# Optimization experiments

Hardware: AMD Instinct MI355X
Metric: run time of the kernel (lower is better)

The kernel has to match this reference:

```python
import jax, jax.numpy as jnp
import numpy as np

B, T, W = 128, 256, 256
D, C, K = 128, 256, 12
TEMP = 0.1


def _l2norm(x):
    # matches F.normalize(dim=-1, eps=1e-12)
    return x / jnp.maximum(jnp.linalg.norm(x, axis=-1, keepdims=True), 1e-12)


def setup_inputs() -> dict:
    key = jax.random.key(0)
    ks = jax.random.split(key, 12)
    s = 0.02
    return {
        "rr_windows": jax.random.normal(ks[0], (B, T, W), dtype=jnp.float32),
        # Encoder: 2-layer MLP window->2D->D
        "enc_w1": jax.random.normal(ks[1], (W, 2 * D), dtype=jnp.float32) * s,
        "enc_b1": jnp.zeros((2 * D,), dtype=jnp.float32),
        "enc_w2": jax.random.normal(ks[2], (2 * D, D), dtype=jnp.float32) * s,
        "enc_b2": jnp.zeros((D,), dtype=jnp.float32),
        # ARBlock: single-layer GRU latent->context
        "W_ih": jax.random.normal(ks[3], (3 * C, D), dtype=jnp.float32) * s,
        "W_hh": jax.random.normal(ks[4], (3 * C, C), dtype=jnp.float32) * s,
        "b_ih": jnp.zeros((3 * C,), dtype=jnp.float32),
        "b_hh": jnp.zeros((3 * C,), dtype=jnp.float32),
        # K prediction heads Wk: context->latent
        "Wk_w": jax.random.normal(ks[5], (K, C, D), dtype=jnp.float32) * s,
        "Wk_b": jnp.zeros((K, D), dtype=jnp.float32),
    }


def _gru(z_seq, W_ih, W_hh, b_ih, b_hh):
    # z_seq: [B, T, D] -> c_seq [B, T, C]
    gx = jnp.einsum("btd,gd->btg", z_seq, W_ih) + b_ih  # [B,T,3C]
    gx = jnp.swapaxes(gx, 0, 1)  # [T,B,3C]
    h0 = jnp.zeros((z_seq.shape[0], C), dtype=z_seq.dtype)

    def step(h, gx_t):
        gh = h @ W_hh.T + b_hh
        xr, xz, xn = jnp.split(gx_t, 3, axis=-1)
        hr, hz, hn = jnp.split(gh, 3, axis=-1)
        r = jax.nn.sigmoid(xr + hr)
        zg = jax.nn.sigmoid(xz + hz)
        n = jnp.tanh(xn + r * hn)
        h_new = (1.0 - zg) * n + zg * h
        return h_new, h_new

    _, hs = jax.lax.scan(step, h0, gx)  # [T,B,C]
    return jnp.swapaxes(hs, 0, 1)


def reference(rr_windows, enc_w1, enc_b1, enc_w2, enc_b2, W_ih, W_hh, b_ih, b_hh, Wk_w, Wk_b):
    # Encoder on each window (dropout inactive)
    h = jax.nn.relu(jnp.einsum("btw,wh->bth", rr_windows, enc_w1) + enc_b1)
    z_seq = jnp.einsum("bth,hd->btd", h, enc_w2) + enc_b2  # [B,T,D]
    z_seq = _l2norm(z_seq)
    c_seq = _gru(z_seq, W_ih, W_hh, b_ih, b_hh)  # [B,T,C]

    Tp = T - K
    c_used = c_seq[:, :Tp, :]  # [B,Tp,C]
    # all (t,k) predictions at once: [K,B,Tp,D]
    preds = _l2norm(jnp.einsum("btc,kcd->kbtd", c_used, Wk_w) + Wk_b[:, None, None, :])
    # logits over ALL timesteps; cat([pos, negs-excl-pos]) == full set reordered,
    # so cross_entropy = logsumexp(full) - pos_logit (logsumexp order-invariant)
    logits = jnp.einsum("kbtd,bsd->kbts", preds, z_seq) / TEMP  # [K,B,Tp,T]
    pos_idx = jnp.arange(Tp)[None, :] + jnp.arange(1, K + 1)[:, None]  # [K,Tp]
    pos_logit = jnp.take_along_axis(
        logits, pos_idx[:, None, :, None], axis=-1
    )[..., 0]  # [K,B,Tp]
    avg_loss = jnp.mean(jax.nn.logsumexp(logits, axis=-1) - pos_logit)

    # accuracy: positive beats all negatives (ties to positive, as in argmax w/ pos first)
    is_pos = jnp.arange(T)[None, None, None, :] == pos_idx[:, None, :, None]
    neg_max = jnp.max(jnp.where(is_pos, -jnp.inf, logits), axis=-1)
    avg_accuracy = jnp.mean((pos_logit >= neg_max).astype(jnp.float32)) * 100.0
    return (avg_loss, avg_accuracy, z_seq, c_seq)
```

## Files before the change

### kernel.cpp

```cpp
#include <hip/hip_runtime.h>
#include <stdint.h>


typedef _Float16 f16;
typedef __attribute__((ext_vector_type(2))) _Float16 f16x2;
typedef __attribute__((ext_vector_type(8))) _Float16 f16x8;
typedef __attribute__((ext_vector_type(4))) float f32x4;

__device__ __forceinline__ f16x2 u2h(unsigned int x) { return __builtin_bit_cast(f16x2, x); }
__device__ __forceinline__ float sigm_(float x) { return __builtin_amdgcn_rcpf(1.f + __expf(-x)); }
__device__ __forceinline__ float tanh_(float x) { return 1.f - 2.f * __builtin_amdgcn_rcpf(__expf(2.f * x) + 1.f); }

#define NTOT_LOSS 374784.0f

__global__ void k_prep(const float* __restrict__ w1, const float* __restrict__ w2,
                       const float* __restrict__ wih, const float* __restrict__ whh,
                       const float* __restrict__ wkw,
                       f16* __restrict__ w1T, f16* __restrict__ w2T, f16* __restrict__ wihF,
                       f16* __restrict__ whhF, f16* __restrict__ wkT, float* __restrict__ accb) {
  const int stride = gridDim.x * blockDim.x;
  const int tid = blockIdx.x * blockDim.x + threadIdx.x;
  if (tid == 0) { accb[0] = 0.f; accb[1] = 0.f; }
  for (int i = tid; i < 65536; i += stride) { int n = i >> 8, k = i & 255; w1T[i] = (f16)w1[k * 256 + n]; }
  for (int i = tid; i < 32768; i += stride) { int n = i >> 8, k = i & 255; w2T[i] = (f16)w2[k * 128 + n]; }
  for (int i = tid; i < 98304; i += stride) wihF[i] = (f16)wih[i];
  for (int i = tid; i < 196608; i += stride) whhF[i] = (f16)whh[i];
  for (int i = tid; i < 393216; i += stride) {
    int kk = i >> 15, rem = i & 32767, d = rem >> 8, c = rem & 255;
    wkT[i] = (f16)wkw[(kk << 15) + c * 128 + d];
  }
}

template <int KTOT, bool AF32, bool RELU>
__global__ __launch_bounds__(256) void k_gemm64(const void* __restrict__ Aptr,
                                                const f16* __restrict__ BT,
                                                const float* __restrict__ bias,
                                                f16* __restrict__ out, const int NT) {
  __shared__ __align__(16) f16 Al[64][40];
  __shared__ __align__(16) f16 Bl[64][40];
  const int m0 = blockIdx.x * 64;
  const int n0 = blockIdx.y * 64;
  const int t = threadIdx.x;
  const int w = t >> 6, l = t & 63, lr = l & 15, lg = l >> 4;
  const int arow = t >> 2, akq = (t & 3) * 8;
  f32x4 acc[4] = {};
  for (int ks = 0; ks < KTOT / 32; ++ks) {
    const int kc = ks * 32;
    __syncthreads();
    if constexpr (AF32) {
      const float* src = (const float*)Aptr + (size_t)(m0 + arow) * KTOT + kc + akq;
      float4 v0 = *(const float4*)src;
      float4 v1 = *(const float4*)(src + 4);
      f16x8 hv = {(f16)v0.x, (f16)v0.y, (f16)v0.z, (f16)v0.w,
                  (f16)v1.x, (f16)v1.y, (f16)v1.z, (f16)v1.w};
      *(f16x8*)&Al[arow][akq] = hv;
    } else {
      const f16* src = (const f16*)Aptr + (size_t)(m0 + arow) * KTOT + kc + akq;
      *(f16x8*)&Al[arow][akq] = *(const f16x8*)src;
    }
    *(f16x8*)&Bl[arow][akq] = *(const f16x8*)(BT + (size_t)(n0 + arow) * KTOT + kc + akq);
    __syncthreads();
    f16x8 af = *(const f16x8*)&Al[16 * w + lr][lg * 8];
#pragma unroll
    for (int nt = 0; nt < 4; ++nt) {
      f16x8 bf = *(const f16x8*)&Bl[nt * 16 + lr][lg * 8];
      acc[nt] = __builtin_amdgcn_mfma_f32_16x16x32_f16(af, bf, acc[nt], 0, 0, 0);
    }
  }
#pragma unroll
  for (int nt = 0; nt < 4; ++nt) {
    const int n = n0 + nt * 16 + lr;
    const float bb = bias[n];
#pragma unroll
    for (int r = 0; r < 4; ++r) {
      const int m = m0 + 16 * w + lg * 4 + r;
      float v = acc[nt][r] + bb;
      if (RELU) v = fmaxf(v, 0.f);
      out[(size_t)m * NT + n] = (f16)v;
    }
  }
}

__global__ __launch_bounds__(256) void k_enc2(const f16* __restrict__ A, const f16* __restrict__ BT,
                                              const float* __restrict__ bias,
                                              float* __restrict__ zf32, f16* __restrict__ zf16) {
  __shared__ __align__(16) f16 Al[64][40];
  __shared__ __align__(16) f16 Bl[128][40];
  const int m0 = blockIdx.x * 64;
  const int t = threadIdx.x;
  const int w = t >> 6, l = t & 63, lr = l & 15, lg = l >> 4;
  const int arow = t >> 2, akq = (t & 3) * 8;
  f32x4 acc[8] = {};
  for (int ks = 0; ks < 8; ++ks) {
    const int kc = ks * 32;
    __syncthreads();
    *(f16x8*)&Al[arow][akq] = *(const f16x8*)(A + (size_t)(m0 + arow) * 256 + kc + akq);
#pragma unroll
    for (int hh = 0; hh < 2; ++hh) {
      const int brow = arow + 64 * hh;
      *(f16x8*)&Bl[brow][akq] = *(const f16x8*)(BT + (size_t)brow * 256 + kc + akq);
    }
    __syncthreads();
    f16x8 af = *(const f16x8*)&Al[16 * w + lr][lg * 8];
#pragma unroll
    for (int nt = 0; nt < 8; ++nt) {
      f16x8 bf = *(const f16x8*)&Bl[nt * 16 + lr][lg * 8];
      acc[nt] = __builtin_amdgcn_mfma_f32_16x16x32_f16(af, bf, acc[nt], 0, 0, 0);
    }
  }
  float v[8][4];
#pragma unroll
  for (int nt = 0; nt < 8; ++nt) {
    const float bb = bias[nt * 16 + lr];
#pragma unroll
    for (int r = 0; r < 4; ++r) v[nt][r] = acc[nt][r] + bb;
  }
#pragma unroll
  for (int r = 0; r < 4; ++r) {
    float ss = 0.f;
#pragma unroll
    for (int nt = 0; nt < 8; ++nt) ss += v[nt][r] * v[nt][r];
    ss += __shfl_xor(ss, 1); ss += __shfl_xor(ss, 2); ss += __shfl_xor(ss, 4); ss += __shfl_xor(ss, 8);
    const float scl = 1.f / fmaxf(sqrtf(ss), 1e-12f);
    const int m = m0 + 16 * w + lg * 4 + r;
#pragma unroll
    for (int nt = 0; nt < 8; ++nt) {
      const int n = nt * 16 + lr;
      const float z = v[nt][r] * scl;
      zf32[(size_t)m * 128 + n] = z;
      zf16[(size_t)m * 128 + n] = (f16)z;
    }
  }
}

__global__ __launch_bounds__(768, 3) void k_gru(const f16* __restrict__ gx, const f16* __restrict__ whh,
                                                const float* __restrict__ bhh,
                                                float* __restrict__ cout, f16* __restrict__ cf16) {
  __shared__ __align__(16) f16 h_lds[2][256];
  __shared__ float rz[2][256];
  const int b = blockIdx.x;
  const int o = threadIdx.x;
  const int g = o >> 8;
  const int c = o & 255;
  uint4 wv[32];
  {
    const uint4* wp = (const uint4*)(whh + (size_t)o * 256);
#pragma unroll
    for (int i = 0; i < 32; ++i) wv[i] = wp[i];
  }
  const float bh = bhh[o];
  if (o < 256) h_lds[0][o] = (f16)0.f;
  float h_own = 0.f;
  const f16* gxp = gx + (size_t)b * 256 * 768 + o;
  float* coutp = cout + (size_t)b * 256 * 256 + c;
  f16* cfp = cf16 + (size_t)b * 256 * 256 + c;
  __syncthreads();
#pragma unroll 1
  for (int tt = 0; tt < 256; ++tt) {
    const int cur = tt & 1;
    const float gxv = (float)gxp[tt * 768];
    float a0 = 0.f, a1 = 0.f, a2 = 0.f, a3 = 0.f;
    const uint4* hp = (const uint4*)(&h_lds[cur][0]);
#pragma unroll
    for (int i = 0; i < 32; ++i) {
      const uint4 hv = hp[i];
      a0 = __builtin_amdgcn_fdot2(u2h(wv[i].x), u2h(hv.x), a0, false);
      a1 = __builtin_amdgcn_fdot2(u2h(wv[i].y), u2h(hv.y), a1, false);
      a2 = __builtin_amdgcn_fdot2(u2h(wv[i].z), u2h(hv.z), a2, false);
      a3 = __builtin_amdgcn_fdot2(u2h(wv[i].w), u2h(hv.w), a3, false);
    }
    const float dot = (a0 + a1) + (a2 + a3) + bh;
    if (g < 2) rz[g][c] = sigm_(gxv + dot);
    __syncthreads();
    if (g == 2) {
      const float r = rz[0][c], zz = rz[1][c];
      const float n = tanh_(gxv + r * dot);
      const float hn = (1.f - zz) * n + zz * h_own;
      h_own = hn;
      h_lds[cur ^ 1][c] = (f16)hn;
      coutp[tt * 256] = hn;
      cfp[tt * 256] = (f16)hn;
    }
    __syncthreads();
  }
}

__global__ __launch_bounds__(256) void k_cpc(const f16* __restrict__ cf16, const f16* __restrict__ zf16,
                                             const f16* __restrict__ wkT, const float* __restrict__ wkb,
                                             float* __restrict__ accb) {
  __shared__ __align__(16) f16 SMc[64 * 264];
  __shared__ __align__(16) f16 Bl[128][40];
  __shared__ __align__(16) f16 P[64][136];
  __shared__ float red[2];
  const int tc = blockIdx.x, b = blockIdx.y, kk = blockIdx.z;
  const int t0 = tc * 64;
  const int t = threadIdx.x;
  const int w = t >> 6, l = t & 63, lr = l & 15, lg = l >> 4;
  {
    const uint32_t* src = (const uint32_t*)(cf16 + ((size_t)b * 256 + t0) * 256);
    uint32_t* dst = (uint32_t*)SMc;
#pragma unroll
    for (int it = 0; it < 32; ++it) {
      const int idx = it * 256 + t, row = idx >> 7, cw = idx & 127;
      dst[row * 132 + cw] = src[row * 128 + cw];
    }
  }
  f32x4 acc[8] = {};
  for (int ks = 0; ks < 8; ++ks) {
    __syncthreads();
    {
      const uint32_t* bsrc = (const uint32_t*)(wkT + ((size_t)kk << 15));
      uint32_t* bd = (uint32_t*)Bl;
#pragma unroll
      for (int it = 0; it < 8; ++it) {
        const int idx = it * 256 + t, row = idx >> 4, kw = idx & 15;
        bd[row * 20 + kw] = bsrc[row * 128 + ks * 16 + kw];
      }
    }
    __syncthreads();
    f16x8 af = *(const f16x8*)&SMc[(16 * w + lr) * 264 + ks * 32 + lg * 8];
#pragma unroll
    for (int nt = 0; nt < 8; ++nt) {
      f16x8 bf = *(const f16x8*)&Bl[nt * 16 + lr][lg * 8];
      acc[nt] = __builtin_amdgcn_mfma_f32_16x16x32_f16(af, bf, acc[nt], 0, 0, 0);
    }
  }
  {
    float v[8][4];
#pragma unroll
    for (int nt = 0; nt < 8; ++nt) {
      const float bb = wkb[kk * 128 + nt * 16 + lr];
#pragma unroll
      for (int r = 0; r < 4; ++r) v[nt][r] = acc[nt][r] + bb;
    }
#pragma unroll
    for (int r = 0; r < 4; ++r) {
      float ss = 0.f;
#pragma unroll
      for (int nt = 0; nt < 8; ++nt) ss += v[nt][r] * v[nt][r];
      ss += __shfl_xor(ss, 1); ss += __shfl_xor(ss, 2); ss += __shfl_xor(ss, 4); ss += __shfl_xor(ss, 8);
      const float scl = 1.f / fmaxf(sqrtf(ss), 1e-12f);
#pragma unroll
      for (int nt = 0; nt < 8; ++nt)
        P[16 * w + lg * 4 + r][nt * 16 + lr] = (f16)(v[nt][r] * scl);
    }
  }
  __syncthreads();
  float m_run[4], s_run[4], pos_v[4], neg_m[4];
#pragma unroll
  for (int r = 0; r < 4; ++r) { m_run[r] = -1e30f; s_run[r] = 0.f; pos_v[r] = -1e30f; neg_m[r] = -1e30f; }
  for (int sc = 0; sc < 4; ++sc) {
    __syncthreads();
    {
      const uint32_t* zsrc = (const uint32_t*)(zf16 + ((size_t)b * 256 + sc * 64) * 128);
      uint32_t* zd = (uint32_t*)SMc;
#pragma unroll
      for (int it = 0; it < 16; ++it) {
        const int idx = it * 256 + t, row = idx >> 6, cw = idx & 63;
        zd[row * 68 + cw] = zsrc[row * 64 + cw];
      }
    }
    __syncthreads();
    f32x4 sa[4] = {};
#pragma unroll
    for (int ks = 0; ks < 4; ++ks) {
      f16x8 af = *(const f16x8*)&P[16 * w + lr][ks * 32 + lg * 8];
#pragma unroll
      for (int nt = 0; nt < 4; ++nt) {
        f16x8 bf = *(const f16x8*)&SMc[(nt * 16 + lr) * 136 + ks * 32 + lg * 8];
        sa[nt] = __builtin_amdgcn_mfma_f32_16x16x32_f16(af, bf, sa[nt], 0, 0, 0);
      }
    }
#pragma unroll
    for (int r = 0; r < 4; ++r) {
      const int trow = t0 + 16 * w + lg * 4 + r;
      const int pos_s = trow + kk + 1;
      float vv[4];
#pragma unroll
      for (int nt = 0; nt < 4; ++nt) vv[nt] = sa[nt][r] * 10.f;
      float cm = fmaxf(fmaxf(vv[0], vv[1]), fmaxf(vv[2], vv[3]));
      cm = fmaxf(cm, __shfl_xor(cm, 1)); cm = fmaxf(cm, __shfl_xor(cm, 2));
      cm = fmaxf(cm, __shfl_xor(cm, 4)); cm = fmaxf(cm, __shfl_xor(cm, 8));
      const float nm = fmaxf(m_run[r], cm);
      float ps = __expf(vv[0] - nm) + __expf(vv[1] - nm) + __expf(vv[2] - nm) + __expf(vv[3] - nm);
      ps += __shfl_xor(ps, 1); ps += __shfl_xor(ps, 2); ps += __shfl_xor(ps, 4); ps += __shfl_xor(ps, 8);
      s_run[r] = s_run[r] * __expf(m_run[r] - nm) + ps;
      m_run[r] = nm;
      const int sbase = sc * 64 + lr;
#pragma unroll
      for (int nt = 0; nt < 4; ++nt) {
        const int s = sbase + nt * 16;
        if (s == pos_s) pos_v[r] = vv[nt];
        else neg_m[r] = fmaxf(neg_m[r], vv[nt]);
      }
    }
  }
  __syncthreads();
  if (t == 0) { red[0] = 0.f; red[1] = 0.f; }
  __syncthreads();
  float lsum = 0.f, csum = 0.f;
#pragma unroll
  for (int r = 0; r < 4; ++r) {
    float pv = pos_v[r], ng = neg_m[r];
    pv = fmaxf(pv, __shfl_xor(pv, 1)); pv = fmaxf(pv, __shfl_xor(pv, 2));
    pv = fmaxf(pv, __shfl_xor(pv, 4)); pv = fmaxf(pv, __shfl_xor(pv, 8));
    ng = fmaxf(ng, __shfl_xor(ng, 1)); ng = fmaxf(ng, __shfl_xor(ng, 2));
    ng = fmaxf(ng, __shfl_xor(ng, 4)); ng = fmaxf(ng, __shfl_xor(ng, 8));
    const int trow = t0 + 16 * w + lg * 4 + r;
    if (lr == 0 && trow < 244) {
      const float lse = m_run[r] + __logf(s_run[r]);
      lsum += lse - pv;
      csum += (pv >= ng) ? 1.f : 0.f;
    }
  }
  if (lr == 0) { atomicAdd(&red[0], lsum); atomicAdd(&red[1], csum); }
  __syncthreads();
  if (t == 0) { atomicAdd(&accb[0], red[0]); atomicAdd(&accb[1], red[1]); }
}

__global__ void k_fin(const float* __restrict__ accb, float* __restrict__ out) {
  out[0] = accb[0] * (1.0f / NTOT_LOSS);
  out[1] = accb[1] * (100.0f / NTOT_LOSS);
}

extern "C" void kernel_launch(void* const* d_in, const int* in_sizes, int n_in,
                              void* d_out, int out_size, void* d_ws, size_t ws_size,
                              hipStream_t stream) {
  (void)in_sizes; (void)n_in; (void)out_size; (void)ws_size;
  const float* rr  = (const float*)d_in[0];
  const float* w1  = (const float*)d_in[1];
  const float* b1  = (const float*)d_in[2];
  const float* w2  = (const float*)d_in[3];
  const float* b2  = (const float*)d_in[4];
  const float* wih = (const float*)d_in[5];
  const float* whh = (const float*)d_in[6];
  const float* bih = (const float*)d_in[7];
  const float* bhh = (const float*)d_in[8];
  const float* wkw = (const float*)d_in[9];
  const float* wkb = (const float*)d_in[10];
  float* out = (float*)d_out;
  char* ws = (char*)d_ws;

  const size_t GX_B = (size_t)32768 * 768 * 2;
  f16* gx   = (f16*)ws;
  f16* h1   = (f16*)ws;
  f16* zf16 = (f16*)(ws + GX_B);
  f16* cf16 = (f16*)(ws + GX_B + 8388608);
  f16* w1T  = (f16*)(ws + GX_B + 8388608 + 16777216);
  f16* w2T  = w1T + 65536;
  f16* wihF = w2T + 32768;
  f16* whhF = wihF + 98304;
  f16* wkT  = whhF + 196608;
  float* accb = (float*)(wkT + 393216);

  float* zf32 = out + 2;
  float* cf32 = out + 2 + 4194304;

  k_prep<<<256, 256, 0, stream>>>(w1, w2, wih, whh, wkw, w1T, w2T, wihF, whhF, wkT, accb);
  k_gemm64<256, true, true><<<dim3(512, 4), 256, 0, stream>>>(rr, w1T, b1, h1, 256);
  k_enc2<<<dim3(512), 256, 0, stream>>>(h1, w2T, b2, zf32, zf16);
  k_gemm64<128, false, false><<<dim3(512, 12), 256, 0, stream>>>(zf16, wihF, bih, gx, 768);
  k_gru<<<128, 768, 0, stream>>>(gx, whhF, bhh, cf32, cf16);
  k_cpc<<<dim3(4, 128, 12), 256, 0, stream>>>(cf16, zf16, wkT, wkb, accb);
  k_fin<<<1, 1, 0, stream>>>(accb, out);
}
```

Before: 592.0 us.

## Compute all three GRU gates per thread to drop the intra-step barrier

The GRU kernel now runs 256 threads per batch row, and each thread computes the r, z and n gate dot products for its own hidden unit. Previously 768 threads each computed one gate. This removes the LDS exchange of r/z values and one __syncthreads per timestep, and each h chunk read from LDS is reused across three gates. W_hh is repacked in the prep kernel into an interleaved layout so the per-thread 384-VGPR weight loads coalesce. The trade-off is heavy register pressure (waves_per_eu 1) and a third as many threads per step, so fewer waves are available to hide latency.

```diff
diff --git a/kernel.cpp b/kernel.cpp
--- a/kernel.cpp
+++ b/kernel.cpp
@@ -6,6 +6,7 @@
 typedef __attribute__((ext_vector_type(2))) _Float16 f16x2;
 typedef __attribute__((ext_vector_type(8))) _Float16 f16x8;
 typedef __attribute__((ext_vector_type(4))) float f32x4;
+typedef __attribute__((ext_vector_type(4))) unsigned int u32x4;
 
 __device__ __forceinline__ f16x2 u2h(unsigned int x) { return __builtin_bit_cast(f16x2, x); }
 __device__ __forceinline__ float sigm_(float x) { return __builtin_amdgcn_rcpf(1.f + __expf(-x)); }
@@ -17,14 +18,17 @@
                        const float* __restrict__ wih, const float* __restrict__ whh,
                        const float* __restrict__ wkw,
                        f16* __restrict__ w1T, f16* __restrict__ w2T, f16* __restrict__ wihF,
-                       f16* __restrict__ whhF, f16* __restrict__ wkT, float* __restrict__ accb) {
+                       f16* __restrict__ whhG, f16* __restrict__ wkT, float* __restrict__ accb) {
   const int stride = gridDim.x * blockDim.x;
   const int tid = blockIdx.x * blockDim.x + threadIdx.x;
   if (tid == 0) { accb[0] = 0.f; accb[1] = 0.f; }
   for (int i = tid; i < 65536; i += stride) { int n = i >> 8, k = i & 255; w1T[i] = (f16)w1[k * 256 + n]; }
   for (int i = tid; i < 32768; i += stride) { int n = i >> 8, k = i & 255; w2T[i] = (f16)w2[k * 128 + n]; }
   for (int i = tid; i < 98304; i += stride) wihF[i] = (f16)wih[i];
-  for (int i = tid; i < 196608; i += stride) whhF[i] = (f16)whh[i];
+  for (int i = tid; i < 196608; i += stride) {
+    int j = i / 6144, rem = i - j * 6144, row = rem >> 3, e = rem & 7;
+    whhG[i] = (f16)whh[row * 256 + j * 8 + e];
+  }
   for (int i = tid; i < 393216; i += stride) {
     int kk = i >> 15, rem = i & 32767, d = rem >> 8, c = rem & 255;
     wkT[i] = (f16)wkw[(kk << 15) + c * 128 + d];
@@ -133,54 +137,73 @@
   }
 }
 
-__global__ __launch_bounds__(768, 3) void k_gru(const f16* __restrict__ gx, const f16* __restrict__ whh,
-                                                const float* __restrict__ bhh,
-                                                float* __restrict__ cout, f16* __restrict__ cf16) {
+__global__ __attribute__((amdgpu_flat_work_group_size(256, 256), amdgpu_waves_per_eu(1, 1)))
+void k_gru(const f16* __restrict__ gx, const f16* __restrict__ whhG,
+           const float* __restrict__ bhh,
+           float* __restrict__ cout, f16* __restrict__ cf16) {
   __shared__ __align__(16) f16 h_lds[2][256];
-  __shared__ float rz[2][256];
   const int b = blockIdx.x;
-  const int o = threadIdx.x;
-  const int g = o >> 8;
-  const int c = o & 255;
-  uint4 wv[32];
+  const int t = threadIdx.x;
+  u32x4 W[96];
   {
-    const uint4* wp = (const uint4*)(whh + (size_t)o * 256);
-#pragma unroll
-    for (int i = 0; i < 32; ++i) wv[i] = wp[i];
-  }
-  const float bh = bhh[o];
-  if (o < 256) h_lds[0][o] = (f16)0.f;
+#pragma unroll
+    for (int j = 0; j < 32; ++j)
+      W[j] = *(const u32x4*)(whhG + ((size_t)j * 768 + t) * 8);
+#pragma unroll
+    for (int j = 0; j < 32; ++j)
+      W[32 + j] = *(const u32x4*)(whhG + ((size_t)j * 768 + 256 + t) * 8);
+#pragma unroll
+    for (int j = 0; j < 32; ++j)
+      W[64 + j] = *(const u32x4*)(whhG + ((size_t)j * 768 + 512 + t) * 8);
+  }
+  const float bhr = bhh[t], bhz = bhh[256 + t], bhn = bhh[512 + t];
+  h_lds[0][t] = (f16)0.f;
   float h_own = 0.f;
-  const f16* gxp = gx + (size_t)b * 256 * 768 + o;
-  float* coutp = cout + (size_t)b * 256 * 256 + c;
-  f16* cfp = cf16 + (size_t)b * 256 * 256 + c;
+  const f16* gxp = gx + (size_t)b * 256 * 768 + t;
+  float* coutp = cout + (size_t)b * 256 * 256 + t;
+  f16* cfp = cf16 + (size_t)b * 256 * 256 + t;
   __syncthreads();
 #pragma unroll 1
   for (int tt = 0; tt < 256; ++tt) {
     const int cur = tt & 1;
-    const float gxv = (float)gxp[tt * 768];
-    float a0 = 0.f, a1 = 0.f, a2 = 0.f, a3 = 0.f;
-    const uint4* hp = (const uint4*)(&h_lds[cur][0]);
-#pragma unroll
-    for (int i = 0; i < 32; ++i) {
-      const uint4 hv = hp[i];
-      a0 = __builtin_amdgcn_fdot2(u2h(wv[i].x), u2h(hv.x), a0, false);
-      a1 = __builtin_amdgcn_fdot2(u2h(wv[i].y), u2h(hv.y), a1, false);
-      a2 = __builtin_amdgcn_fdot2(u2h(wv[i].z), u2h(hv.z), a2, false);
-      a3 = __builtin_amdgcn_fdot2(u2h(wv[i].w), u2h(hv.w), a3, false);
-    }
-    const float dot = (a0 + a1) + (a2 + a3) + bh;
-    if (g < 2) rz[g][c] = sigm_(gxv + dot);
-    __syncthreads();
-    if (g == 2) {
-      const float r = rz[0][c], zz = rz[1][c];
-      const float n = tanh_(gxv + r * dot);
-      const float hn = (1.f - zz) * n + zz * h_own;
-      h_own = hn;
-      h_lds[cur ^ 1][c] = (f16)hn;
-      coutp[tt * 256] = hn;
-      cfp[tt * 256] = (f16)hn;
-    }
+    const float gxr = (float)gxp[tt * 768];
+    const float gxz = (float)gxp[tt * 768 + 256];
+    const float gxn = (float)gxp[tt * 768 + 512];
+    float ar0 = 0.f, ar1 = 0.f, az0 = 0.f, az1 = 0.f, an0 = 0.f, an1 = 0.f;
+    const u32x4* hp = (const u32x4*)(&h_lds[cur][0]);
+#pragma unroll
+    for (int q = 0; q < 8; ++q) {
+      u32x4 hq[4];
+#pragma unroll
+      for (int j = 0; j < 4; ++j) hq[j] = hp[q * 4 + j];
+#pragma unroll
+      for (int j = 0; j < 4; ++j) {
+        const int w = q * 4 + j;
+        ar0 = __builtin_amdgcn_fdot2(u2h(W[w][0]), u2h(hq[j][0]), ar0, false);
+        ar1 = __builtin_amdgcn_fdot2(u2h(W[w][1]), u2h(hq[j][1]), ar1, false);
+        ar0 = __builtin_amdgcn_fdot2(u2h(W[w][2]), u2h(hq[j][2]), ar0, false);
+        ar1 = __builtin_amdgcn_fdot2(u2h(W[w][3]), u2h(hq[j][3]), ar1, false);
+        az0 = __builtin_amdgcn_fdot2(u2h(W[32 + w][0]), u2h(hq[j][0]), az0, false);
+        az1 = __builtin_amdgcn_fdot2(u2h(W[32 + w][1]), u2h(hq[j][1]), az1, false);
+        az0 = __builtin_amdgcn_fdot2(u2h(W[32 + w][2]), u2h(hq[j][2]), az0, false);
+        az1 = __builtin_amdgcn_fdot2(u2h(W[32 + w][3]), u2h(hq[j][3]), az1, false);
+        an0 = __builtin_amdgcn_fdot2(u2h(W[64 + w][0]), u2h(hq[j][0]), an0, false);
+        an1 = __builtin_amdgcn_fdot2(u2h(W[64 + w][1]), u2h(hq[j][1]), an1, false);
+        an0 = __builtin_amdgcn_fdot2(u2h(W[64 + w][2]), u2h(hq[j][2]), an0, false);
+        an1 = __builtin_amdgcn_fdot2(u2h(W[64 + w][3]), u2h(hq[j][3]), an1, false);
+      }
+    }
+    const float dr = ar0 + ar1 + bhr;
+    const float dz = az0 + az1 + bhz;
+    const float dn = an0 + an1 + bhn;
+    const float r = sigm_(gxr + dr);
+    const float zz = sigm_(gxz + dz);
+    const float n = tanh_(gxn + r * dn);
+    const float hn = (1.f - zz) * n + zz * h_own;
+    h_own = hn;
+    h_lds[cur ^ 1][t] = (f16)hn;
+    coutp[tt * 256] = hn;
+    cfp[tt * 256] = (f16)hn;
     __syncthreads();
   }
 }
@@ -349,18 +372,18 @@
   f16* w1T  = (f16*)(ws + GX_B + 8388608 + 16777216);
   f16* w2T  = w1T + 65536;
   f16* wihF = w2T + 32768;
-  f16* whhF = wihF + 98304;
-  f16* wkT  = whhF + 196608;
+  f16* whhG = wihF + 98304;
+  f16* wkT  = whhG + 196608;
   float* accb = (float*)(wkT + 393216);
 
   float* zf32 = out + 2;
   float* cf32 = out + 2 + 4194304;
 
-  k_prep<<<256, 256, 0, stream>>>(w1, w2, wih, whh, wkw, w1T, w2T, wihF, whhF, wkT, accb);
+  k_prep<<<256, 256, 0, stream>>>(w1, w2, wih, whh, wkw, w1T, w2T, wihF, whhG, wkT, accb);
   k_gemm64<256, true, true><<<dim3(512, 4), 256, 0, stream>>>(rr, w1T, b1, h1, 256);
   k_enc2<<<dim3(512), 256, 0, stream>>>(h1, w2T, b2, zf32, zf16);
   k_gemm64<128, false, false><<<dim3(512, 12), 256, 0, stream>>>(zf16, wihF, bih, gx, 768);
-  k_gru<<<128, 768, 0, stream>>>(gx, whhF, bhh, cf32, cf16);
+  k_gru<<<128, 256, 0, stream>>>(gx, whhG, bhh, cf32, cf16);
   k_cpc<<<dim3(4, 128, 12), 256, 0, stream>>>(cf16, zf16, wkT, wkb, accb);
   k_fin<<<1, 1, 0, stream>>>(accb, out);
 }
```

After: 880.6 us. 48.8% more time.

## Batch GRU recurrence over 16 sequences per block using MFMA

Applied to the files above, without the earlier changes.

The GRU kernel moves from one block per sequence doing fp16 dot2 products to 8 blocks, each processing 16 batch rows with MFMA 16x16x32 and W_hh held in registers in a fragment-swizzled layout. The input-gate bias and the r/z hidden biases are pre-summed into the gx GEMM, and gx is written in a layout matching each lane's MFMA fragments. The fp32 context output is now produced by a separate conversion kernel from the fp16 hidden state. The hidden state is carried in fp16 between steps, which may slightly change numerics, and only 8 CUs stay busy during the long serial recurrence.

```diff
diff --git a/kernel.cpp b/kernel.cpp
--- a/kernel.cpp
+++ b/kernel.cpp
@@ -15,23 +15,33 @@
 
 __global__ void k_prep(const float* __restrict__ w1, const float* __restrict__ w2,
                        const float* __restrict__ wih, const float* __restrict__ whh,
-                       const float* __restrict__ wkw,
+                       const float* __restrict__ wkw, const float* __restrict__ bih,
+                       const float* __restrict__ bhh,
                        f16* __restrict__ w1T, f16* __restrict__ w2T, f16* __restrict__ wihF,
-                       f16* __restrict__ whhF, f16* __restrict__ wkT, float* __restrict__ accb) {
+                       f16* __restrict__ whhG2, f16* __restrict__ wkT,
+                       float* __restrict__ biasc, float* __restrict__ accb) {
   const int stride = gridDim.x * blockDim.x;
   const int tid = blockIdx.x * blockDim.x + threadIdx.x;
   if (tid == 0) { accb[0] = 0.f; accb[1] = 0.f; }
+  for (int i = tid; i < 768; i += stride) biasc[i] = bih[i] + (i < 512 ? bhh[i] : 0.f);
   for (int i = tid; i < 65536; i += stride) { int n = i >> 8, k = i & 255; w1T[i] = (f16)w1[k * 256 + n]; }
   for (int i = tid; i < 32768; i += stride) { int n = i >> 8, k = i & 255; w2T[i] = (f16)w2[k * 128 + n]; }
   for (int i = tid; i < 98304; i += stride) wihF[i] = (f16)wih[i];
-  for (int i = tid; i < 196608; i += stride) whhF[i] = (f16)whh[i];
+  for (int i = tid; i < 196608; i += stride) {
+    const int e = i & 7, lane = (i >> 3) & 63, rest = i >> 9;
+    const int w = rest / 96, fidx = rest % 96;
+    const int ks = fidx & 7, gnt = fidx >> 3, g = gnt >> 2, nt = gnt & 3;
+    const int row = g * 256 + w * 64 + nt * 16 + (lane & 15);
+    const int k = ks * 32 + (lane >> 4) * 8 + e;
+    whhG2[i] = (f16)whh[row * 256 + k];
+  }
   for (int i = tid; i < 393216; i += stride) {
     int kk = i >> 15, rem = i & 32767, d = rem >> 8, c = rem & 255;
     wkT[i] = (f16)wkw[(kk << 15) + c * 128 + d];
   }
 }
 
-template <int KTOT, bool AF32, bool RELU>
+template <int KTOT, bool AF32, bool RELU, bool GXS>
 __global__ __launch_bounds__(256) void k_gemm64(const void* __restrict__ Aptr,
                                                 const f16* __restrict__ BT,
                                                 const float* __restrict__ bias,
@@ -76,7 +86,16 @@
       const int m = m0 + 16 * w + lg * 4 + r;
       float v = acc[nt][r] + bb;
       if (RELU) v = fmaxf(v, 0.f);
-      out[(size_t)m * NT + n] = (f16)v;
+      if constexpr (GXS) {
+        const int b = m >> 8, tt2 = m & 255, bc = b >> 4, ml = b & 15;
+        const int g = n >> 8, col = n & 255;
+        const int wv = col >> 6, nt2 = (col >> 4) & 3, cl2 = col & 15;
+        const int lane2 = ((ml >> 2) << 4) | cl2;
+        const int slot = g * 16 + nt2 * 4 + (ml & 3);
+        out[((((size_t)bc * 256 + tt2) * 4 + wv) * 64 + lane2) * 48 + slot] = (f16)v;
+      } else {
+        out[(size_t)m * NT + n] = (f16)v;
+      }
     }
   }
 }
@@ -133,56 +152,76 @@
   }
 }
 
-__global__ __launch_bounds__(768, 3) void k_gru(const f16* __restrict__ gx, const f16* __restrict__ whh,
-                                                const float* __restrict__ bhh,
-                                                float* __restrict__ cout, f16* __restrict__ cf16) {
-  __shared__ __align__(16) f16 h_lds[2][256];
-  __shared__ float rz[2][256];
-  const int b = blockIdx.x;
-  const int o = threadIdx.x;
-  const int g = o >> 8;
-  const int c = o & 255;
-  uint4 wv[32];
+__global__ __attribute__((amdgpu_flat_work_group_size(256, 256), amdgpu_waves_per_eu(1, 1)))
+void k_gru(const f16* __restrict__ gxS, const f16* __restrict__ whhG2,
+           const float* __restrict__ bhh, f16* __restrict__ cf16) {
+  __shared__ __align__(16) f16 h_lds[2][16][264];
+  const int bc = blockIdx.x;
+  const int t = threadIdx.x;
+  const int w = t >> 6, lane = t & 63;
+  const int hi = lane >> 4, cl = lane & 15;
+  f16x8 Wf[96];
   {
-    const uint4* wp = (const uint4*)(whh + (size_t)o * 256);
-#pragma unroll
-    for (int i = 0; i < 32; ++i) wv[i] = wp[i];
-  }
-  const float bh = bhh[o];
-  if (o < 256) h_lds[0][o] = (f16)0.f;
-  float h_own = 0.f;
-  const f16* gxp = gx + (size_t)b * 256 * 768 + o;
-  float* coutp = cout + (size_t)b * 256 * 256 + c;
-  f16* cfp = cf16 + (size_t)b * 256 * 256 + c;
+    const f16* base = whhG2 + ((size_t)w * 96) * 512 + (size_t)lane * 8;
+#pragma unroll
+    for (int f = 0; f < 96; ++f) Wf[f] = *(const f16x8*)(base + (size_t)f * 512);
+  }
+  float bhn[4];
+#pragma unroll
+  for (int nt = 0; nt < 4; ++nt) bhn[nt] = bhh[512 + 64 * w + nt * 16 + cl];
+  for (int idx = t; idx < 16 * 264; idx += 256) h_lds[0][idx / 264][idx % 264] = (f16)0.f;
+  const f16* gxp = gxS + ((((size_t)bc * 256) * 4 + w) * 64 + lane) * 48;
+  f16* cfb = cf16 + ((size_t)(bc * 16 + 4 * hi) << 16) + 64 * w + cl;
   __syncthreads();
 #pragma unroll 1
   for (int tt = 0; tt < 256; ++tt) {
     const int cur = tt & 1;
-    const float gxv = (float)gxp[tt * 768];
-    float a0 = 0.f, a1 = 0.f, a2 = 0.f, a3 = 0.f;
-    const uint4* hp = (const uint4*)(&h_lds[cur][0]);
-#pragma unroll
-    for (int i = 0; i < 32; ++i) {
-      const uint4 hv = hp[i];
-      a0 = __builtin_amdgcn_fdot2(u2h(wv[i].x), u2h(hv.x), a0, false);
-      a1 = __builtin_amdgcn_fdot2(u2h(wv[i].y), u2h(hv.y), a1, false);
-      a2 = __builtin_amdgcn_fdot2(u2h(wv[i].z), u2h(hv.z), a2, false);
-      a3 = __builtin_amdgcn_fdot2(u2h(wv[i].w), u2h(hv.w), a3, false);
-    }
-    const float dot = (a0 + a1) + (a2 + a3) + bh;
-    if (g < 2) rz[g][c] = sigm_(gxv + dot);
-    __syncthreads();
-    if (g == 2) {
-      const float r = rz[0][c], zz = rz[1][c];
-      const float n = tanh_(gxv + r * dot);
-      const float hn = (1.f - zz) * n + zz * h_own;
-      h_own = hn;
-      h_lds[cur ^ 1][c] = (f16)hn;
-      coutp[tt * 256] = hn;
-      cfp[tt * 256] = (f16)hn;
-    }
-    __syncthreads();
-  }
+    const f16* gxt = gxp + (size_t)tt * 12288;
+    uint4 gxv[6];
+#pragma unroll
+    for (int j = 0; j < 6; ++j) gxv[j] = *(const uint4*)(gxt + j * 8);
+    f16 hold[4][4];
+#pragma unroll
+    for (int nt = 0; nt < 4; ++nt)
+#pragma unroll
+      for (int i = 0; i < 4; ++i)
+        hold[nt][i] = h_lds[cur][4 * hi + i][64 * w + nt * 16 + cl];
+    f32x4 acc[12] = {};
+#pragma unroll
+    for (int ks = 0; ks < 8; ++ks) {
+      const f16x8 af = *(const f16x8*)&h_lds[cur][cl][ks * 32 + hi * 8];
+#pragma unroll
+      for (int gn = 0; gn < 12; ++gn)
+        acc[gn] = __builtin_amdgcn_mfma_f32_16x16x32_f16(af, Wf[gn * 8 + ks], acc[gn], 0, 0, 0);
+    }
+#pragma unroll
+    for (int nt = 0; nt < 4; ++nt) {
+#pragma unroll
+      for (int i = 0; i < 4; ++i) {
+        const int sr = nt * 4 + i, sz = 16 + nt * 4 + i, sn = 32 + nt * 4 + i;
+        const float xr = (float)u2h(gxv[sr >> 3][(sr >> 1) & 3])[sr & 1];
+        const float xz = (float)u2h(gxv[sz >> 3][(sz >> 1) & 3])[sz & 1];
+        const float xn = (float)u2h(gxv[sn >> 3][(sn >> 1) & 3])[sn & 1];
+        const float r = sigm_(xr + acc[nt][i]);
+        const float z = sigm_(xz + acc[4 + nt][i]);
+        const float n = tanh_(xn + r * (acc[8 + nt][i] + bhn[nt]));
+        const float h = (1.f - z) * n + z * (float)hold[nt][i];
+        const f16 hh = (f16)h;
+        h_lds[cur ^ 1][4 * hi + i][64 * w + nt * 16 + cl] = hh;
+        cfb[((size_t)i << 16) + (size_t)tt * 256 + nt * 16] = hh;
+      }
+    }
+    __syncthreads();
+  }
+}
+
+__global__ void k_c32(const f16* __restrict__ cf, float* __restrict__ o) {
+  const size_t i = (size_t)(blockIdx.x * blockDim.x + threadIdx.x) * 8;
+  const f16x8 v = *(const f16x8*)(cf + i);
+  float4 a = {(float)v[0], (float)v[1], (float)v[2], (float)v[3]};
+  float4 b = {(float)v[4], (float)v[5], (float)v[6], (float)v[7]};
+  *(float4*)(o + i) = a;
+  *(float4*)(o + i + 4) = b;
 }
 
 __global__ __launch_bounds__(256) void k_cpc(const f16* __restrict__ cf16, const f16* __restrict__ zf16,
@@ -342,25 +381,28 @@
   char* ws = (char*)d_ws;
 
   const size_t GX_B = (size_t)32768 * 768 * 2;
-  f16* gx   = (f16*)ws;
+  f16* gxS  = (f16*)ws;
   f16* h1   = (f16*)ws;
   f16* zf16 = (f16*)(ws + GX_B);
   f16* cf16 = (f16*)(ws + GX_B + 8388608);
   f16* w1T  = (f16*)(ws + GX_B + 8388608 + 16777216);
   f16* w2T  = w1T + 65536;
   f16* wihF = w2T + 32768;
-  f16* whhF = wihF + 98304;
-  f16* wkT  = whhF + 196608;
-  float* accb = (float*)(wkT + 393216);
+  f16* whhG2 = wihF + 98304;
+  f16* wkT  = whhG2 + 196608;
+  float* biasc = (float*)(wkT + 393216);
+  float* accb  = biasc + 768;
 
   float* zf32 = out + 2;
   float* cf32 = out + 2 + 4194304;
 
-  k_prep<<<256, 256, 0, stream>>>(w1, w2, wih, whh, wkw, w1T, w2T, wihF, whhF, wkT, accb);
-  k_gemm64<256, true, true><<<dim3(512, 4), 256, 0, stream>>>(rr, w1T, b1, h1, 256);
+  k_prep<<<256, 256, 0, stream>>>(w1, w2, wih, whh, wkw, bih, bhh,
+                                  w1T, w2T, wihF, whhG2, wkT, biasc, accb);
+  k_gemm64<256, true, true, false><<<dim3(512, 4), 256, 0, stream>>>(rr, w1T, b1, h1, 256);
   k_enc2<<<dim3(512), 256, 0, stream>>>(h1, w2T, b2, zf32, zf16);
-  k_gemm64<128, false, false><<<dim3(512, 12), 256, 0, stream>>>(zf16, wihF, bih, gx, 768);
-  k_gru<<<128, 768, 0, stream>>>(gx, whhF, bhh, cf32, cf16);
+  k_gemm64<128, false, false, true><<<dim3(512, 12), 256, 0, stream>>>(zf16, wihF, biasc, gxS, 768);
+  k_gru<<<8, 256, 0, stream>>>(gxS, whhG2, bhh, cf16);
+  k_c32<<<4096, 256, 0, stream>>>(cf16, cf32);
   k_cpc<<<dim3(4, 128, 12), 256, 0, stream>>>(cf16, zf16, wkT, wkb, accb);
   k_fin<<<1, 1, 0, stream>>>(accb, out);
 }
```

Result: slower. 1.152 ms (+94.6%).

## Quantize GRU recurrent weights and hidden state to int8 with sdot4

Applied to the files above, without the earlier changes.

Replaces the fp16 W_hh register-resident weights and fp16 hidden state in the GRU recurrence with per-row int8 weights (stored interleaved in global memory, read each step) and an int8-quantized hidden state, using sdot4 integer dot products rescaled by a per-row scale. This frees the 32 uint4 registers each thread held for weights and halves the LDS footprint of h. The trade-off is re-reading weights from cache every timestep and a real loss of precision in the recurrence: quantizing h to 1/127 steps and weights to int8 may drift c_seq beyond tolerance.

```diff
diff --git a/kernel.cpp b/kernel.cpp
--- a/kernel.cpp
+++ b/kernel.cpp
@@ -17,14 +17,36 @@
                        const float* __restrict__ wih, const float* __restrict__ whh,
                        const float* __restrict__ wkw,
                        f16* __restrict__ w1T, f16* __restrict__ w2T, f16* __restrict__ wihF,
-                       f16* __restrict__ whhF, f16* __restrict__ wkT, float* __restrict__ accb) {
+                       uint8_t* __restrict__ whhQ, float* __restrict__ wsc,
+                       f16* __restrict__ wkT, float* __restrict__ accb) {
   const int stride = gridDim.x * blockDim.x;
   const int tid = blockIdx.x * blockDim.x + threadIdx.x;
   if (tid == 0) { accb[0] = 0.f; accb[1] = 0.f; }
   for (int i = tid; i < 65536; i += stride) { int n = i >> 8, k = i & 255; w1T[i] = (f16)w1[k * 256 + n]; }
   for (int i = tid; i < 32768; i += stride) { int n = i >> 8, k = i & 255; w2T[i] = (f16)w2[k * 128 + n]; }
   for (int i = tid; i < 98304; i += stride) wihF[i] = (f16)wih[i];
-  for (int i = tid; i < 196608; i += stride) whhF[i] = (f16)whh[i];
+  if (tid < 768) {
+    const float* row = whh + (size_t)tid * 256;
+    float amax = 0.f;
+    for (int k = 0; k < 256; ++k) amax = fmaxf(amax, fabsf(row[k]));
+    const float s = fmaxf(amax, 1e-20f) / 127.f;
+    const float rs = 127.f / fmaxf(amax, 1e-20f);
+    wsc[tid] = s / 127.f;
+    for (int jq = 0; jq < 16; ++jq) {
+      uint32_t words[4];
+      for (int w32 = 0; w32 < 4; ++w32) {
+        uint32_t p = 0;
+        for (int e = 0; e < 4; ++e) {
+          const int k = jq * 16 + w32 * 4 + e;
+          const int q = (int)rintf(row[k] * rs);
+          p |= ((uint32_t)(uint8_t)(int8_t)q) << (8 * e);
+        }
+        words[w32] = p;
+      }
+      *(uint4*)(whhQ + ((size_t)jq * 768 + tid) * 16) =
+          make_uint4(words[0], words[1], words[2], words[3]);
+    }
+  }
   for (int i = tid; i < 393216; i += stride) {
     int kk = i >> 15, rem = i & 32767, d = rem >> 8, c = rem & 255;
     wkT[i] = (f16)wkw[(kk << 15) + c * 128 + d];
@@ -133,43 +155,40 @@
   }
 }
 
-__global__ __launch_bounds__(768, 3) void k_gru(const f16* __restrict__ gx, const f16* __restrict__ whh,
-                                                const float* __restrict__ bhh,
+__global__ __launch_bounds__(768, 3) void k_gru(const f16* __restrict__ gx, const uint8_t* __restrict__ whhQ,
+                                                const float* __restrict__ wsc, const float* __restrict__ bhh,
                                                 float* __restrict__ cout, f16* __restrict__ cf16) {
-  __shared__ __align__(16) f16 h_lds[2][256];
+  __shared__ __align__(16) uint32_t h8[2][64];
   __shared__ float rz[2][256];
   const int b = blockIdx.x;
   const int o = threadIdx.x;
   const int g = o >> 8;
   const int c = o & 255;
-  uint4 wv[32];
-  {
-    const uint4* wp = (const uint4*)(whh + (size_t)o * 256);
-#pragma unroll
-    for (int i = 0; i < 32; ++i) wv[i] = wp[i];
-  }
+  const float sc = wsc[o];
   const float bh = bhh[o];
-  if (o < 256) h_lds[0][o] = (f16)0.f;
+  if (o < 64) { h8[0][o] = 0u; }
   float h_own = 0.f;
   const f16* gxp = gx + (size_t)b * 256 * 768 + o;
   float* coutp = cout + (size_t)b * 256 * 256 + c;
   f16* cfp = cf16 + (size_t)b * 256 * 256 + c;
+  const uint8_t* wbase = whhQ + (size_t)o * 16;
   __syncthreads();
 #pragma unroll 1
   for (int tt = 0; tt < 256; ++tt) {
     const int cur = tt & 1;
     const float gxv = (float)gxp[tt * 768];
-    float a0 = 0.f, a1 = 0.f, a2 = 0.f, a3 = 0.f;
-    const uint4* hp = (const uint4*)(&h_lds[cur][0]);
-#pragma unroll
-    for (int i = 0; i < 32; ++i) {
-      const uint4 hv = hp[i];
-      a0 = __builtin_amdgcn_fdot2(u2h(wv[i].x), u2h(hv.x), a0, false);
-      a1 = __builtin_amdgcn_fdot2(u2h(wv[i].y), u2h(hv.y), a1, false);
-      a2 = __builtin_amdgcn_fdot2(u2h(wv[i].z), u2h(hv.z), a2, false);
-      a3 = __builtin_amdgcn_fdot2(u2h(wv[i].w), u2h(hv.w), a3, false);
-    }
-    const float dot = (a0 + a1) + (a2 + a3) + bh;
+    int i0 = 0, i1 = 0, i2 = 0, i3 = 0;
+    const uint4* hp = (const uint4*)(&h8[cur][0]);
+#pragma unroll
+    for (int jq = 0; jq < 16; ++jq) {
+      const uint4 wq = *(const uint4*)(wbase + (size_t)jq * 12288);
+      const uint4 hq = hp[jq];
+      i0 = __builtin_amdgcn_sdot4((int)wq.x, (int)hq.x, i0, false);
+      i1 = __builtin_amdgcn_sdot4((int)wq.y, (int)hq.y, i1, false);
+      i2 = __builtin_amdgcn_sdot4((int)wq.z, (int)hq.z, i2, false);
+      i3 = __builtin_amdgcn_sdot4((int)wq.w, (int)hq.w, i3, false);
+    }
+    const float dot = (float)((i0 + i1) + (i2 + i3)) * sc + bh;
     if (g < 2) rz[g][c] = sigm_(gxv + dot);
     __syncthreads();
     if (g == 2) {
@@ -177,7 +196,8 @@
       const float n = tanh_(gxv + r * dot);
       const float hn = (1.f - zz) * n + zz * h_own;
       h_own = hn;
-      h_lds[cur ^ 1][c] = (f16)hn;
+      const int qh = (int)rintf(hn * 127.f);
+      ((uint8_t*)&h8[cur ^ 1][0])[c] = (uint8_t)(int8_t)qh;
       coutp[tt * 256] = hn;
       cfp[tt * 256] = (f16)hn;
     }
@@ -349,18 +369,19 @@
   f16* w1T  = (f16*)(ws + GX_B + 8388608 + 16777216);
   f16* w2T  = w1T + 65536;
   f16* wihF = w2T + 32768;
-  f16* whhF = wihF + 98304;
-  f16* wkT  = whhF + 196608;
+  uint8_t* whhQ = (uint8_t*)(wihF + 98304);
+  float* wsc = (float*)(whhQ + 196608);
+  f16* wkT  = (f16*)(wsc + 768);
   float* accb = (float*)(wkT + 393216);
 
   float* zf32 = out + 2;
   float* cf32 = out + 2 + 4194304;
 
-  k_prep<<<256, 256, 0, stream>>>(w1, w2, wih, whh, wkw, w1T, w2T, wihF, whhF, wkT, accb);
+  k_prep<<<256, 256, 0, stream>>>(w1, w2, wih, whh, wkw, w1T, w2T, wihF, whhQ, wsc, wkT, accb);
   k_gemm64<256, true, true><<<dim3(512, 4), 256, 0, stream>>>(rr, w1T, b1, h1, 256);
   k_enc2<<<dim3(512), 256, 0, stream>>>(h1, w2T, b2, zf32, zf16);
   k_gemm64<128, false, false><<<dim3(512, 12), 256, 0, stream>>>(zf16, wihF, bih, gx, 768);
-  k_gru<<<128, 768, 0, stream>>>(gx, whhF, bhh, cf32, cf16);
+  k_gru<<<128, 768, 0, stream>>>(gx, whhQ, wsc, bhh, cf32, cf16);
   k_cpc<<<dim3(4, 128, 12), 256, 0, stream>>>(cf16, zf16, wkT, wkb, accb);
   k_fin<<<1, 1, 0, stream>>>(accb, out);
 }
```

After: 504.4 us. 1.17x faster.
